# Optimization experiments

Measured on AMD Instinct MI355X. Metric: run time of the kernel, lower is better.

Reference implementation:

```python
import jax, jax.numpy as jnp
import numpy as np
import math

N_HEAD, D_HEAD, D_MODEL = 12, 64, 768
ATT_SPAN = 512            # max_position_embeddings // stride**block_index
SCALE_FACTOR = 3          # 1 + 2 (relative attention: content + c2p + p2c)
CLS_TOKENS = 1            # num_highway_cls_tokens + 1
INF = 1e6
LN_EPS = 1e-5
SCALE = 1.0 / (math.sqrt(D_HEAD) * math.sqrt(SCALE_FACTOR))


def setup_inputs() -> dict:
    key = jax.random.key(0)
    ks = jax.random.split(key, 10)
    B, S = 2, 2048
    lin = lambda k, shape: jax.random.normal(k, shape, dtype=jnp.float32) * 0.02
    return {
        "query": jax.random.normal(ks[0], (B, S, D_MODEL), dtype=jnp.float32),
        "attention_mask": jnp.ones((B, S), dtype=jnp.float32),
        "pos_key_embed": jax.random.normal(ks[1], (2 * ATT_SPAN, D_MODEL), dtype=jnp.float32),
        "pos_query_embed": jax.random.normal(ks[2], (2 * ATT_SPAN, D_MODEL), dtype=jnp.float32),
        "Wq": lin(ks[3], (N_HEAD * D_HEAD, D_MODEL)),
        "bq": jnp.zeros((N_HEAD * D_HEAD,), dtype=jnp.float32),
        "Wk": lin(ks[4], (N_HEAD * D_HEAD, D_MODEL)),
        "Wv": lin(ks[5], (D_MODEL, D_MODEL)),
        "bv": jnp.zeros((D_MODEL,), dtype=jnp.float32),
        "Wpq": lin(ks[6], (N_HEAD * D_HEAD, D_MODEL)),
        "bpq": jnp.zeros((N_HEAD * D_HEAD,), dtype=jnp.float32),
        "Wpk": lin(ks[7], (N_HEAD * D_HEAD, D_MODEL)),
        "r_w_bias": jax.random.normal(ks[8], (N_HEAD, D_HEAD), dtype=jnp.float32) * 0.02,
        "ln_gamma": jnp.ones((D_MODEL,), dtype=jnp.float32),
        "ln_beta": jnp.zeros((D_MODEL,), dtype=jnp.float32),
    }


def _forward(query, attention_mask, pos_key_embed, pos_query_embed,
             Wq, bq, Wk, Wv, bv, Wpq, bpq, Wpk, r_w_bias, ln_gamma, ln_beta):
    B, S, _ = query.shape
    # self-attention: key = value = query
    v = query @ Wv.T + bv                                             # v_head projection
    qh = (query @ Wq.T + bq).reshape(B, S, N_HEAD, D_HEAD)
    kh = (query @ Wk.T).reshape(B, S, N_HEAD, D_HEAD)
    vh = v.reshape(B, S, N_HEAD, D_MODEL // N_HEAD)
    qh = (qh + r_w_bias) * SCALE                                       # bias + scale fused into q

    content = jnp.einsum('bind,bjnd->bnij', qh, kh)                    # [B,n,S,S]

    # ---- disentangled relative-position bias (DeBERTa-style c2p + p2c) ----
    pos_k = (pos_key_embed @ Wpk.T).reshape(2 * ATT_SPAN, N_HEAD, D_HEAD).transpose(1, 0, 2)          # [n,2span,d]
    pos_q = (pos_query_embed @ Wpq.T + bpq).reshape(2 * ATT_SPAN, N_HEAD, D_HEAD).transpose(1, 0, 2)  # [n,2span,d]
    qbn = qh.transpose(0, 2, 1, 3)                                     # [B,n,S,d] (already scaled)
    kbn = kh.transpose(0, 2, 1, 3)
    rel = jnp.arange(S)[:, None] - jnp.arange(S)[None, :]              # [S,S] query - key

    # content -> position
    c2p = jnp.einsum('bnid,njd->bnij', qbn, pos_k)                     # [B,n,S,2span]
    c2p_idx = jnp.clip(rel + ATT_SPAN, 0, 2 * ATT_SPAN - 1)
    c2p_score = jnp.take_along_axis(c2p, c2p_idx[None, None], axis=-1) # [B,n,S,S]

    # position -> content
    p2c = jnp.einsum('bnjd,nid->bnji', kbn * (1.0 / math.sqrt(D_HEAD * SCALE_FACTOR)), pos_q)  # [B,n,S,2span]
    p2c_idx = jnp.clip(-rel + ATT_SPAN, 0, 2 * ATT_SPAN - 1)
    p2c_score = jnp.take_along_axis(p2c, p2c_idx[None, None], axis=-1).swapaxes(-1, -2)        # [B,n,S,S]

    bias = c2p_score + p2c_score
    # zero out bias on cls rows and cls columns (the padding/concat trick in the source)
    keep = (jnp.arange(S) >= CLS_TOKENS).astype(bias.dtype)
    bias = bias * (keep[:, None] * keep[None, :])

    score = content + bias
    score = score - INF * (1.0 - attention_mask[:, None, None, :])
    prob = jax.nn.softmax(score, axis=-1)                              # attention_dropout = 0.0

    attn_vec = jnp.einsum('bnij,bjnd->bind', prob, vh).reshape(B, S, D_MODEL)
    # fused residual + LayerNorm(attn_out)
    mu = attn_vec.mean(-1, keepdims=True)
    var = ((attn_vec - mu) ** 2).mean(-1, keepdims=True)
    ln = (attn_vec - mu) / jnp.sqrt(var + LN_EPS) * ln_gamma + ln_beta
    return query + ln


def reference(query, attention_mask, pos_key_embed, pos_query_embed,
              Wq, bq, Wk, Wv, bv, Wpq, bpq, Wpk, r_w_bias, ln_gamma, ln_beta):
    return _forward(query, attention_mask, pos_key_embed, pos_query_embed,
                    Wq, bq, Wk, Wv, bv, Wpq, bpq, Wpk, r_w_bias, ln_gamma, ln_beta)
```

## Files before the change

kernel.cpp:

```cpp
#include <hip/hip_runtime.h>
#include <math.h>

#define NB     2
#define SEQ    2048
#define NHEAD  12
#define DMODEL 768
#define SPAN2  1024
#define SCALEF 0.07216878364870323f

typedef unsigned short ushort;
typedef unsigned int   uint;
typedef __attribute__((ext_vector_type(8))) short  bh8;
typedef __attribute__((ext_vector_type(4))) float  f32x4;
typedef __attribute__((ext_vector_type(4))) unsigned short us4;

__device__ inline ushort f2bf(float x) {
    uint u = __builtin_bit_cast(uint, x);
    u += 0x7FFFu + ((u >> 16) & 1u);
    return (ushort)(u >> 16);
}
__device__ inline float b2f(ushort h) {
    uint u = ((uint)h) << 16;
    return __builtin_bit_cast(float, u);
}

__device__ __forceinline__ void gld16(const ushort* g, ushort* l) {
    __builtin_amdgcn_global_load_lds(
        (const __attribute__((address_space(1))) void*)g,
        (__attribute__((address_space(3))) void*)l, 16, 0, 0);
}

__device__ __forceinline__ bh8 ldsfrag(const ushort* tile, int row, int slot) {
    return *(const bh8*)((const char*)tile + row * 128 + (((slot ^ (row & 7)) << 4)));
}

struct CvtArgs {
    const float* src[8];
    ushort*      dst[8];
    int          n[8];
};

__global__ __launch_bounds__(256) void cvt_bf16(CvtArgs a)
{
    const int seg = blockIdx.y;
    const int i   = (blockIdx.x * 256 + threadIdx.x) * 8;
    if (i >= a.n[seg]) return;
    const float4* s = (const float4*)(a.src[seg] + i);
    const float4 x = s[0], y = s[1];
    bh8 o;
    o[0] = (short)f2bf(x.x); o[1] = (short)f2bf(x.y);
    o[2] = (short)f2bf(x.z); o[3] = (short)f2bf(x.w);
    o[4] = (short)f2bf(y.x); o[5] = (short)f2bf(y.y);
    o[6] = (short)f2bf(y.z); o[7] = (short)f2bf(y.w);
    *(bh8*)(a.dst[seg] + i) = o;
}

__global__ __launch_bounds__(256) void proj_mfma2(
    const ushort* __restrict__ X, const ushort* __restrict__ W,
    const float* __restrict__ b1, const float* __restrict__ b2,
    float scale, int rowsPerBatch,
    ushort* __restrict__ out, ushort* __restrict__ outT)
{
    __shared__ ushort Xs[32 * 64];
    __shared__ ushort Ws[64 * 64];
    const int r0 = blockIdx.x * 32;
    const int n  = blockIdx.y;
    const int c0 = n * 64;
    const int tid  = threadIdx.x;
    const int w    = tid >> 6;
    const int lane = tid & 63;
    const int lo   = lane & 15;
    const int hi8  = (lane >> 4) * 8;
    const int g4   = (lane >> 4) * 4;
    const int wr   = w & 1;
    const int wc   = w >> 1;
    const int r8   = lane >> 3;
    const int sl   = lane & 7;

    f32x4 acc[2] = {};
    for (int k0 = 0; k0 < DMODEL; k0 += 64) {
        {
            const int r = w * 8 + r8;
            const int s = sl ^ (r & 7);
            gld16(X + (size_t)(r0 + r) * DMODEL + k0 + s * 8, Xs + w * 512);
        }
        #pragma unroll
        for (int i = 0; i < 2; ++i) {
            const int c = i * 4 + w;
            const int r = c * 8 + r8;
            const int s = sl ^ (r & 7);
            gld16(W + (size_t)(c0 + r) * DMODEL + k0 + s * 8, Ws + c * 512);
        }
        __syncthreads();
        const bh8 a0 = ldsfrag(Xs, wr * 16 + lo, hi8 >> 3);
        const bh8 a1 = ldsfrag(Xs, wr * 16 + lo, 4 + (hi8 >> 3));
        #pragma unroll
        for (int ct = 0; ct < 2; ++ct) {
            const int row = wc * 32 + ct * 16 + lo;
            const bh8 wb0 = ldsfrag(Ws, row, hi8 >> 3);
            const bh8 wb1 = ldsfrag(Ws, row, 4 + (hi8 >> 3));
            acc[ct] = __builtin_amdgcn_mfma_f32_16x16x32_bf16(a0, wb0, acc[ct], 0, 0, 0);
            acc[ct] = __builtin_amdgcn_mfma_f32_16x16x32_bf16(a1, wb1, acc[ct], 0, 0, 0);
        }
        __syncthreads();
    }

    const int rbase = r0 + wr * 16 + g4;
    const int bb  = rbase / rowsPerBatch;
    const int rr0 = rbase - bb * rowsPerBatch;
    #pragma unroll
    for (int ct = 0; ct < 2; ++ct) {
        const int d = wc * 32 + ct * 16 + lo;
        const int c = c0 + d;
        const float badd = (b1 ? b1[c] : 0.f) + (b2 ? b2[c] : 0.f);
        if (out) {
            #pragma unroll
            for (int reg = 0; reg < 4; ++reg)
                out[(((size_t)bb * NHEAD + n) * rowsPerBatch + rr0 + reg) * 64 + d] =
                    f2bf((acc[ct][reg] + badd) * scale);
        }
        if (outT) {
            us4 o;
            #pragma unroll
            for (int reg = 0; reg < 4; ++reg)
                o[reg] = f2bf((acc[ct][reg] + badd) * scale);
            *(us4*)&outT[(((size_t)bb * NHEAD + n) * 64 + d) * rowsPerBatch + rr0] = o;
        }
    }
}

__global__ __launch_bounds__(256, 3) void attn_mfma8(
    const ushort* __restrict__ qh, const ushort* __restrict__ kh,
    const ushort* __restrict__ vht, const ushort* __restrict__ posk,
    const ushort* __restrict__ posq, const float* __restrict__ mask,
    float* __restrict__ attn)
{
    __shared__ ushort POS[128 * 64];
    __shared__ ushort Kb [64 * 64];
    __shared__ ushort Vb [64 * 64];
    __shared__ ushort T1c[64 * 68];
    __shared__ ushort T2c[64 * 68];

    const int id   = blockIdx.x;
    const int xcd  = id & 7;
    const int slot = id >> 3;
    const int bn   = xcd * 3 + (slot >> 5);
    const int i0   = (slot & 31) * 64;
    const int b    = bn / NHEAD;
    const int n    = bn % NHEAD;

    const int tid  = threadIdx.x;
    const int w    = tid >> 6;
    const int lane = tid & 63;
    const int lo   = lane & 15;
    const int hi8  = (lane >> 4) * 8;
    const int g4   = (lane >> 4) * 4;
    const int w16  = w * 16;
    const int r8   = lane >> 3;
    const int sl   = lane & 7;
    const int slotA = hi8 >> 3;

    const ushort* qrow = qh + ((size_t)bn * SEQ + i0 + w16 + lo) * 64;
    const bh8 qa0 = *(const bh8*)&qrow[hi8];
    const bh8 qa1 = *(const bh8*)&qrow[32 + hi8];

    const ushort* khb = kh   + (size_t)bn * SEQ * 64;
    const ushort* vtb = vht  + (size_t)bn * 64 * SEQ;
    const ushort* pkh = posk + (size_t)n * SPAN2 * 64;
    const ushort* pqh = posq + (size_t)n * SPAN2 * 64;
    const float*  mrw = mask + (size_t)b * SEQ;

    f32x4 accPV[4] = {};
    float mrow[4] = {-1e30f, -1e30f, -1e30f, -1e30f};
    float lrow[4] = {0.f, 0.f, 0.f, 0.f};

    for (int j0 = 0; j0 < SEQ; j0 += 64) {
        const int d0base = i0 - j0 + 449;

        #pragma unroll
        for (int i = 0; i < 2; ++i) {
            const int c = i * 4 + w;
            const int r = c * 8 + r8;
            const int s = sl ^ (r & 7);
            gld16(khb + (size_t)(j0 + r) * 64 + s * 8, Kb + c * 512);
        }
        #pragma unroll
        for (int i = 0; i < 4; ++i) {
            const int c = i * 4 + w;
            const int r = c * 8 + r8;
            const int s = sl ^ (r & 7);
            int gr = d0base + r; gr = gr < 0 ? 0 : (gr > SPAN2 - 1 ? SPAN2 - 1 : gr);
            gld16(pkh + (size_t)gr * 64 + s * 8, POS + c * 512);
        }
        __syncthreads();

        const bh8 ka0 = ldsfrag(Kb, w16 + lo, slotA);
        const bh8 ka1 = ldsfrag(Kb, w16 + lo, 4 + slotA);
        f32x4 z1[5];
        #pragma unroll
        for (int q = 0; q < 5; ++q) {
            const int u1 = (w + q) * 16 + lo;
            const bh8 pk0 = ldsfrag(POS, u1, slotA);
            const bh8 pk1 = ldsfrag(POS, u1, 4 + slotA);
            f32x4 a = {};
            a = __builtin_amdgcn_mfma_f32_16x16x32_bf16(qa0, pk0, a, 0, 0, 0);
            z1[q] = __builtin_amdgcn_mfma_f32_16x16x32_bf16(qa1, pk1, a, 0, 0, 0);
        }
        __syncthreads();

        #pragma unroll
        for (int i = 0; i < 4; ++i) {
            const int c = i * 4 + w;
            const int r = c * 8 + r8;
            const int s = sl ^ (r & 7);
            int gr = d0base + r; gr = gr < 0 ? 0 : (gr > SPAN2 - 1 ? SPAN2 - 1 : gr);
            gld16(pqh + (size_t)gr * 64 + s * 8, POS + c * 512);
        }
        #pragma unroll
        for (int i = 0; i < 2; ++i) {
            const int c = i * 4 + w;
            const int r = c * 8 + r8;
            const int s = sl ^ (r & 7);
            gld16(vtb + (size_t)r * SEQ + j0 + s * 8, Vb + c * 512);
        }
        #pragma unroll
        for (int q = 0; q < 5; ++q)
            #pragma unroll
            for (int reg = 0; reg < 4; ++reg) {
                const int cc2 = q * 16 + lo - g4 - reg;
                if (cc2 >= 0 && cc2 < 64)
                    T1c[(w16 + g4 + reg) * 68 + cc2] = f2bf(z1[q][reg]);
            }
        f32x4 accS[4];
        #pragma unroll
        for (int ct = 0; ct < 4; ++ct) {
            const bh8 kb0 = ldsfrag(Kb, ct * 16 + lo, slotA);
            const bh8 kb1 = ldsfrag(Kb, ct * 16 + lo, 4 + slotA);
            f32x4 z = {};
            z = __builtin_amdgcn_mfma_f32_16x16x32_bf16(qa0, kb0, z, 0, 0, 0);
            accS[ct] = __builtin_amdgcn_mfma_f32_16x16x32_bf16(qa1, kb1, z, 0, 0, 0);
        }
        float maskadd[4];
        #pragma unroll
        for (int ct = 0; ct < 4; ++ct)
            maskadd[ct] = -1e6f * (1.f - mrw[j0 + ct * 16 + lo]);
        __syncthreads();

        #pragma unroll
        for (int q = 0; q < 5; ++q) {
            const int u2 = (3 - w + q) * 16 + lo;
            const bh8 pq0 = ldsfrag(POS, u2, slotA);
            const bh8 pq1 = ldsfrag(POS, u2, 4 + slotA);
            f32x4 z = {};
            z = __builtin_amdgcn_mfma_f32_16x16x32_bf16(ka0, pq0, z, 0, 0, 0);
            z = __builtin_amdgcn_mfma_f32_16x16x32_bf16(ka1, pq1, z, 0, 0, 0);
            #pragma unroll
            for (int reg = 0; reg < 4; ++reg) {
                const int il2 = q * 16 + lo + g4 + reg - 15;
                if (il2 >= 0 && il2 < 64)
                    T2c[(w16 + g4 + reg) * 68 + il2] = f2bf(z[reg]);
            }
        }
        __syncthreads();

        float corr[4];
        char* pbase = (char*)POS + w * 2048;
        #pragma unroll
        for (int reg = 0; reg < 4; ++reg) {
            const int il = w16 + g4 + reg;
            const int gi = i0 + il;
            float s[4], rmax = -1e30f;
            #pragma unroll
            for (int ct = 0; ct < 4; ++ct) {
                const int jl = ct * 16 + lo;
                float v = accS[ct][reg];
                if (gi >= 1 && (j0 + jl) >= 1)
                    v += b2f(T1c[il * 68 + 63 - jl]) + b2f(T2c[jl * 68 + il]);
                v += maskadd[ct];
                s[ct] = v;
                rmax = fmaxf(rmax, v);
            }
            rmax = fmaxf(rmax, __shfl_xor(rmax, 1));
            rmax = fmaxf(rmax, __shfl_xor(rmax, 2));
            rmax = fmaxf(rmax, __shfl_xor(rmax, 4));
            rmax = fmaxf(rmax, __shfl_xor(rmax, 8));
            const float mnew = fmaxf(mrow[reg], rmax);
            const float cc   = __expf(mrow[reg] - mnew);
            float psum = 0.f;
            const int prow = g4 + reg;
            #pragma unroll
            for (int ct = 0; ct < 4; ++ct) {
                const float p = __expf(s[ct] - mnew);
                psum += p;
                *(ushort*)(pbase + prow * 128 + ((((ct * 16 + lo) * 2)) ^ ((prow & 7) * 16))) = f2bf(p);
            }
            psum += __shfl_xor(psum, 1);
            psum += __shfl_xor(psum, 2);
            psum += __shfl_xor(psum, 4);
            psum += __shfl_xor(psum, 8);
            lrow[reg] = lrow[reg] * cc + psum;
            mrow[reg] = mnew;
            corr[reg] = cc;
        }

        {
            const bh8 pa0 = *(const bh8*)(pbase + lo * 128 + ((slotA << 4) ^ ((lo & 7) * 16)));
            const bh8 pa1 = *(const bh8*)(pbase + lo * 128 + (((4 + slotA) << 4) ^ ((lo & 7) * 16)));
            #pragma unroll
            for (int dt = 0; dt < 4; ++dt) {
                const bh8 vb0 = ldsfrag(Vb, dt * 16 + lo, slotA);
                const bh8 vb1 = ldsfrag(Vb, dt * 16 + lo, 4 + slotA);
                f32x4 a = accPV[dt];
                #pragma unroll
                for (int reg = 0; reg < 4; ++reg) a[reg] *= corr[reg];
                a = __builtin_amdgcn_mfma_f32_16x16x32_bf16(pa0, vb0, a, 0, 0, 0);
                accPV[dt] = __builtin_amdgcn_mfma_f32_16x16x32_bf16(pa1, vb1, a, 0, 0, 0);
            }
        }
        __syncthreads();
    }

    #pragma unroll
    for (int reg = 0; reg < 4; ++reg) {
        const int i = i0 + w16 + g4 + reg;
        const float inv = 1.f / lrow[reg];
        #pragma unroll
        for (int dt = 0; dt < 4; ++dt)
            attn[((size_t)b * SEQ + i) * DMODEL + n * 64 + dt * 16 + lo] =
                accPV[dt][reg] * inv;
    }
}

__global__ __launch_bounds__(256) void resid_ln(
    float* __restrict__ attn, const float* __restrict__ query,
    const float* __restrict__ gamma, const float* __restrict__ beta)
{
    const int b = blockIdx.y;
    const int i = blockIdx.x;
    const size_t base = ((size_t)b * SEQ + i) * DMODEL;
    const int tid = threadIdx.x;

    float x[3];
    #pragma unroll
    for (int s = 0; s < 3; ++s) x[s] = attn[base + s * 256 + tid];

    float sum = x[0] + x[1] + x[2];
    float sq  = x[0]*x[0] + x[1]*x[1] + x[2]*x[2];
    #pragma unroll
    for (int off = 32; off; off >>= 1) {
        sum += __shfl_xor(sum, off);
        sq  += __shfl_xor(sq, off);
    }
    __shared__ float red[2][4];
    const int w = tid >> 6;
    if ((tid & 63) == 0) { red[0][w] = sum; red[1][w] = sq; }
    __syncthreads();
    sum = red[0][0] + red[0][1] + red[0][2] + red[0][3];
    sq  = red[1][0] + red[1][1] + red[1][2] + red[1][3];

    const float mu  = sum * (1.f / DMODEL);
    const float var = sq * (1.f / DMODEL) - mu * mu;
    const float inv = rsqrtf(var + 1e-5f);

    #pragma unroll
    for (int s = 0; s < 3; ++s) {
        const int c = s * 256 + tid;
        attn[base + c] = query[base + c] + (x[s] - mu) * inv * gamma[c] + beta[c];
    }
}

extern "C" void kernel_launch(void* const* d_in, const int* in_sizes, int n_in,
                              void* d_out, int out_size, void* d_ws, size_t ws_size,
                              hipStream_t stream)
{
    const float* query = (const float*)d_in[0];
    const float* mask  = (const float*)d_in[1];
    const float* pke   = (const float*)d_in[2];
    const float* pqe   = (const float*)d_in[3];
    const float* Wq    = (const float*)d_in[4];
    const float* bq    = (const float*)d_in[5];
    const float* Wk    = (const float*)d_in[6];
    const float* Wv    = (const float*)d_in[7];
    const float* bv    = (const float*)d_in[8];
    const float* Wpq   = (const float*)d_in[9];
    const float* bpq   = (const float*)d_in[10];
    const float* Wpk   = (const float*)d_in[11];
    const float* rwb   = (const float*)d_in[12];
    const float* gamma = (const float*)d_in[13];
    const float* beta  = (const float*)d_in[14];

    float* out = (float*)d_out;

    const int Q_N  = NB * SEQ * DMODEL;
    const int P_N  = SPAN2 * DMODEL;
    const int W_N  = DMODEL * DMODEL;
    const size_t QKV_ELEMS = (size_t)NB * NHEAD * SEQ * 64;
    const size_t POS_ELEMS = (size_t)NHEAD * SPAN2 * 64;

    ushort* xb   = (ushort*)d_ws;
    ushort* pkeb = xb   + Q_N;
    ushort* pqeb = pkeb + P_N;
    ushort* wqb  = pqeb + P_N;
    ushort* wkb  = wqb  + W_N;
    ushort* wvb  = wkb  + W_N;
    ushort* wpqb = wvb  + W_N;
    ushort* wpkb = wpqb + W_N;
    ushort* qh   = wpkb + W_N;
    ushort* kh   = qh   + QKV_ELEMS;
    ushort* vht  = kh   + QKV_ELEMS;
    ushort* pkp  = vht  + QKV_ELEMS;
    ushort* pqp  = pkp  + POS_ELEMS;

    dim3 blk(256);

    CvtArgs ca;
    ca.src[0] = query; ca.dst[0] = xb;   ca.n[0] = Q_N;
    ca.src[1] = pke;   ca.dst[1] = pkeb; ca.n[1] = P_N;
    ca.src[2] = pqe;   ca.dst[2] = pqeb; ca.n[2] = P_N;
    ca.src[3] = Wq;    ca.dst[3] = wqb;  ca.n[3] = W_N;
    ca.src[4] = Wk;    ca.dst[4] = wkb;  ca.n[4] = W_N;
    ca.src[5] = Wv;    ca.dst[5] = wvb;  ca.n[5] = W_N;
    ca.src[6] = Wpq;   ca.dst[6] = wpqb; ca.n[6] = W_N;
    ca.src[7] = Wpk;   ca.dst[7] = wpkb; ca.n[7] = W_N;
    cvt_bf16<<<dim3((Q_N / 8 + 255) / 256, 8), blk, 0, stream>>>(ca);

    proj_mfma2<<<dim3(128, NHEAD), blk, 0, stream>>>(xb,   wqb,  bq,  rwb, SCALEF, SEQ,   qh,  nullptr);
    proj_mfma2<<<dim3(128, NHEAD), blk, 0, stream>>>(xb,   wkb,  nullptr, nullptr, 1.f, SEQ, kh, nullptr);
    proj_mfma2<<<dim3(128, NHEAD), blk, 0, stream>>>(xb,   wvb,  bv,  nullptr, 1.f,   SEQ,   nullptr, vht);
    proj_mfma2<<<dim3(32,  NHEAD), blk, 0, stream>>>(pkeb, wpkb, nullptr, nullptr, 1.f, SPAN2, pkp, nullptr);
    proj_mfma2<<<dim3(32,  NHEAD), blk, 0, stream>>>(pqeb, wpqb, bpq, nullptr, SCALEF, SPAN2, pqp, nullptr);

    attn_mfma8<<<dim3(NB * NHEAD * (SEQ / 64)), blk, 0, stream>>>(
        qh, kh, vht, pkp, pqp, mask, out);

    resid_ln<<<dim3(SEQ, NB), blk, 0, stream>>>(out, query, gamma, beta);
}
```

Before: 245.5 us.

## Fuse QKV and positional projections; add clamped-tile fast path in attention

Measured after the change: 222.7 us. 1.1x faster.

```diff
diff --git a/kernel.cpp b/kernel.cpp
--- a/kernel.cpp
+++ b/kernel.cpp
@@ -55,14 +55,18 @@
     *(bh8*)(a.dst[seg] + i) = o;
 }
 
-__global__ __launch_bounds__(256) void proj_mfma2(
-    const ushort* __restrict__ X, const ushort* __restrict__ W,
-    const float* __restrict__ b1, const float* __restrict__ b2,
-    float scale, int rowsPerBatch,
-    ushort* __restrict__ out, ushort* __restrict__ outT)
+__global__ __launch_bounds__(256) void proj_qkv(
+    const ushort* __restrict__ X,
+    const ushort* __restrict__ Wq, const ushort* __restrict__ Wk,
+    const ushort* __restrict__ Wv,
+    const float* __restrict__ bq, const float* __restrict__ rwb,
+    const float* __restrict__ bv,
+    ushort* __restrict__ qh, ushort* __restrict__ kh, ushort* __restrict__ vht)
 {
-    __shared__ ushort Xs[32 * 64];
-    __shared__ ushort Ws[64 * 64];
+    __shared__ ushort Xs [32 * 64];
+    __shared__ ushort Wqs[64 * 64];
+    __shared__ ushort Wks[64 * 64];
+    __shared__ ushort Wvs[64 * 64];
     const int r0 = blockIdx.x * 32;
     const int n  = blockIdx.y;
     const int c0 = n * 64;
@@ -76,8 +80,9 @@
     const int wc   = w >> 1;
     const int r8   = lane >> 3;
     const int sl   = lane & 7;
-
-    f32x4 acc[2] = {};
+    const int slotA = hi8 >> 3;
+
+    f32x4 aq[2] = {}, ak[2] = {}, av[2] = {};
     for (int k0 = 0; k0 < DMODEL; k0 += 64) {
         {
             const int r = w * 8 + r8;
@@ -89,47 +94,120 @@
             const int c = i * 4 + w;
             const int r = c * 8 + r8;
             const int s = sl ^ (r & 7);
-            gld16(W + (size_t)(c0 + r) * DMODEL + k0 + s * 8, Ws + c * 512);
-        }
-        __syncthreads();
-        const bh8 a0 = ldsfrag(Xs, wr * 16 + lo, hi8 >> 3);
-        const bh8 a1 = ldsfrag(Xs, wr * 16 + lo, 4 + (hi8 >> 3));
+            gld16(Wq + (size_t)(c0 + r) * DMODEL + k0 + s * 8, Wqs + c * 512);
+            gld16(Wk + (size_t)(c0 + r) * DMODEL + k0 + s * 8, Wks + c * 512);
+            gld16(Wv + (size_t)(c0 + r) * DMODEL + k0 + s * 8, Wvs + c * 512);
+        }
+        __syncthreads();
+        const bh8 a0 = ldsfrag(Xs, wr * 16 + lo, slotA);
+        const bh8 a1 = ldsfrag(Xs, wr * 16 + lo, 4 + slotA);
         #pragma unroll
         for (int ct = 0; ct < 2; ++ct) {
             const int row = wc * 32 + ct * 16 + lo;
-            const bh8 wb0 = ldsfrag(Ws, row, hi8 >> 3);
-            const bh8 wb1 = ldsfrag(Ws, row, 4 + (hi8 >> 3));
-            acc[ct] = __builtin_amdgcn_mfma_f32_16x16x32_bf16(a0, wb0, acc[ct], 0, 0, 0);
-            acc[ct] = __builtin_amdgcn_mfma_f32_16x16x32_bf16(a1, wb1, acc[ct], 0, 0, 0);
+            aq[ct] = __builtin_amdgcn_mfma_f32_16x16x32_bf16(a0, ldsfrag(Wqs, row, slotA),     aq[ct], 0, 0, 0);
+            aq[ct] = __builtin_amdgcn_mfma_f32_16x16x32_bf16(a1, ldsfrag(Wqs, row, 4 + slotA), aq[ct], 0, 0, 0);
+            ak[ct] = __builtin_amdgcn_mfma_f32_16x16x32_bf16(a0, ldsfrag(Wks, row, slotA),     ak[ct], 0, 0, 0);
+            ak[ct] = __builtin_amdgcn_mfma_f32_16x16x32_bf16(a1, ldsfrag(Wks, row, 4 + slotA), ak[ct], 0, 0, 0);
+            av[ct] = __builtin_amdgcn_mfma_f32_16x16x32_bf16(a0, ldsfrag(Wvs, row, slotA),     av[ct], 0, 0, 0);
+            av[ct] = __builtin_amdgcn_mfma_f32_16x16x32_bf16(a1, ldsfrag(Wvs, row, 4 + slotA), av[ct], 0, 0, 0);
         }
         __syncthreads();
     }
 
     const int rbase = r0 + wr * 16 + g4;
-    const int bb  = rbase / rowsPerBatch;
-    const int rr0 = rbase - bb * rowsPerBatch;
+    const int bb  = rbase >> 11;
+    const int rr0 = rbase & (SEQ - 1);
     #pragma unroll
     for (int ct = 0; ct < 2; ++ct) {
         const int d = wc * 32 + ct * 16 + lo;
         const int c = c0 + d;
-        const float badd = (b1 ? b1[c] : 0.f) + (b2 ? b2[c] : 0.f);
-        if (out) {
-            #pragma unroll
-            for (int reg = 0; reg < 4; ++reg)
-                out[(((size_t)bb * NHEAD + n) * rowsPerBatch + rr0 + reg) * 64 + d] =
-                    f2bf((acc[ct][reg] + badd) * scale);
-        }
-        if (outT) {
-            us4 o;
-            #pragma unroll
-            for (int reg = 0; reg < 4; ++reg)
-                o[reg] = f2bf((acc[ct][reg] + badd) * scale);
-            *(us4*)&outT[(((size_t)bb * NHEAD + n) * 64 + d) * rowsPerBatch + rr0] = o;
-        }
-    }
-}
-
-__global__ __launch_bounds__(256, 3) void attn_mfma8(
+        const float bqv = bq[c] + rwb[c];
+        const float bvv = bv[c];
+        us4 o;
+        #pragma unroll
+        for (int reg = 0; reg < 4; ++reg) {
+            const size_t rowi = ((size_t)bb * NHEAD + n) * SEQ + rr0 + reg;
+            qh[rowi * 64 + d] = f2bf((aq[ct][reg] + bqv) * SCALEF);
+            kh[rowi * 64 + d] = f2bf(ak[ct][reg]);
+            o[reg] = f2bf(av[ct][reg] + bvv);
+        }
+        *(us4*)&vht[(((size_t)bb * NHEAD + n) * 64 + d) * SEQ + rr0] = o;
+    }
+}
+
+__global__ __launch_bounds__(256) void proj_pos(
+    const ushort* __restrict__ PKe, const ushort* __restrict__ PQe,
+    const ushort* __restrict__ Wpk, const ushort* __restrict__ Wpq,
+    const float* __restrict__ bpq,
+    ushort* __restrict__ pkp, ushort* __restrict__ pqp)
+{
+    __shared__ ushort Xk [32 * 64];
+    __shared__ ushort Xq [32 * 64];
+    __shared__ ushort Wks[64 * 64];
+    __shared__ ushort Wqs[64 * 64];
+    const int r0 = blockIdx.x * 32;
+    const int n  = blockIdx.y;
+    const int c0 = n * 64;
+    const int tid  = threadIdx.x;
+    const int w    = tid >> 6;
+    const int lane = tid & 63;
+    const int lo   = lane & 15;
+    const int hi8  = (lane >> 4) * 8;
+    const int g4   = (lane >> 4) * 4;
+    const int wr   = w & 1;
+    const int wc   = w >> 1;
+    const int r8   = lane >> 3;
+    const int sl   = lane & 7;
+    const int slotA = hi8 >> 3;
+
+    f32x4 apk[2] = {}, apq[2] = {};
+    for (int k0 = 0; k0 < DMODEL; k0 += 64) {
+        {
+            const int r = w * 8 + r8;
+            const int s = sl ^ (r & 7);
+            gld16(PKe + (size_t)(r0 + r) * DMODEL + k0 + s * 8, Xk + w * 512);
+            gld16(PQe + (size_t)(r0 + r) * DMODEL + k0 + s * 8, Xq + w * 512);
+        }
+        #pragma unroll
+        for (int i = 0; i < 2; ++i) {
+            const int c = i * 4 + w;
+            const int r = c * 8 + r8;
+            const int s = sl ^ (r & 7);
+            gld16(Wpk + (size_t)(c0 + r) * DMODEL + k0 + s * 8, Wks + c * 512);
+            gld16(Wpq + (size_t)(c0 + r) * DMODEL + k0 + s * 8, Wqs + c * 512);
+        }
+        __syncthreads();
+        const bh8 xk0 = ldsfrag(Xk, wr * 16 + lo, slotA);
+        const bh8 xk1 = ldsfrag(Xk, wr * 16 + lo, 4 + slotA);
+        const bh8 xq0 = ldsfrag(Xq, wr * 16 + lo, slotA);
+        const bh8 xq1 = ldsfrag(Xq, wr * 16 + lo, 4 + slotA);
+        #pragma unroll
+        for (int ct = 0; ct < 2; ++ct) {
+            const int row = wc * 32 + ct * 16 + lo;
+            apk[ct] = __builtin_amdgcn_mfma_f32_16x16x32_bf16(xk0, ldsfrag(Wks, row, slotA),     apk[ct], 0, 0, 0);
+            apk[ct] = __builtin_amdgcn_mfma_f32_16x16x32_bf16(xk1, ldsfrag(Wks, row, 4 + slotA), apk[ct], 0, 0, 0);
+            apq[ct] = __builtin_amdgcn_mfma_f32_16x16x32_bf16(xq0, ldsfrag(Wqs, row, slotA),     apq[ct], 0, 0, 0);
+            apq[ct] = __builtin_amdgcn_mfma_f32_16x16x32_bf16(xq1, ldsfrag(Wqs, row, 4 + slotA), apq[ct], 0, 0, 0);
+        }
+        __syncthreads();
+    }
+
+    const int rr0 = r0 + wr * 16 + g4;
+    #pragma unroll
+    for (int ct = 0; ct < 2; ++ct) {
+        const int d = wc * 32 + ct * 16 + lo;
+        const int c = c0 + d;
+        const float badd = bpq[c];
+        #pragma unroll
+        for (int reg = 0; reg < 4; ++reg) {
+            const size_t rowi = ((size_t)n * SPAN2 + rr0 + reg);
+            pkp[rowi * 64 + d] = f2bf(apk[ct][reg]);
+            pqp[rowi * 64 + d] = f2bf((apq[ct][reg] + badd) * SCALEF);
+        }
+    }
+}
+
+__global__ __launch_bounds__(256, 3) void attn_mfma9(
     const ushort* __restrict__ qh, const ushort* __restrict__ kh,
     const ushort* __restrict__ vht, const ushort* __restrict__ posk,
     const ushort* __restrict__ posq, const float* __restrict__ mask,
@@ -140,6 +218,8 @@
     __shared__ ushort Vb [64 * 64];
     __shared__ ushort T1c[64 * 68];
     __shared__ ushort T2c[64 * 68];
+    __shared__ ushort CL [8 * 64];
+    __shared__ float  Crow[2][64];
 
     const int id   = blockIdx.x;
     const int xcd  = id & 7;
@@ -170,13 +250,44 @@
     const ushort* pqh = posq + (size_t)n * SPAN2 * 64;
     const float*  mrw = mask + (size_t)b * SEQ;
 
+    if (w == 0) {
+        const int row = lane >> 3;
+        const int sr  = row & 3;
+        const ushort* src = (sr == 0) ? pkh
+                          : (sr == 1) ? pkh + (size_t)(SPAN2 - 1) * 64
+                          : (sr == 2) ? pqh
+                          :             pqh + (size_t)(SPAN2 - 1) * 64;
+        gld16(src + (lane & 7) * 8, CL);
+    }
+    __syncthreads();
+    {
+        const bh8 p0a = *(const bh8*)&CL[0 * 64 + hi8];
+        const bh8 p0b = *(const bh8*)&CL[0 * 64 + 32 + hi8];
+        const bh8 p1a = *(const bh8*)&CL[1 * 64 + hi8];
+        const bh8 p1b = *(const bh8*)&CL[1 * 64 + 32 + hi8];
+        float c0p = 0.f, c1p = 0.f;
+        #pragma unroll
+        for (int e = 0; e < 8; ++e) {
+            const float q0 = b2f((ushort)qa0[e]);
+            const float q1 = b2f((ushort)qa1[e]);
+            c0p += q0 * b2f((ushort)p0a[e]) + q1 * b2f((ushort)p0b[e]);
+            c1p += q0 * b2f((ushort)p1a[e]) + q1 * b2f((ushort)p1b[e]);
+        }
+        c0p += __shfl_xor(c0p, 16); c0p += __shfl_xor(c0p, 32);
+        c1p += __shfl_xor(c1p, 16); c1p += __shfl_xor(c1p, 32);
+        if (hi8 == 0) { Crow[0][w16 + lo] = c0p; Crow[1][w16 + lo] = c1p; }
+    }
+
     f32x4 accPV[4] = {};
     float mrow[4] = {-1e30f, -1e30f, -1e30f, -1e30f};
     float lrow[4] = {0.f, 0.f, 0.f, 0.f};
 
     for (int j0 = 0; j0 < SEQ; j0 += 64) {
         const int d0base = i0 - j0 + 449;
-
+        const bool clamp0 = (d0base <= -126);
+        const bool clamp1 = (d0base >= 1023);
+
+        if (!clamp0 && !clamp1) {
         #pragma unroll
         for (int i = 0; i < 2; ++i) {
             const int c = i * 4 + w;
@@ -318,6 +429,110 @@
             }
         }
         __syncthreads();
+
+        } else {
+        #pragma unroll
+        for (int i = 0; i < 2; ++i) {
+            const int c = i * 4 + w;
+            const int r = c * 8 + r8;
+            const int s = sl ^ (r & 7);
+            gld16(khb + (size_t)(j0 + r) * 64 + s * 8, Kb + c * 512);
+            gld16(vtb + (size_t)r * SEQ + j0 + s * 8, Vb + c * 512);
+        }
+        __syncthreads();
+
+        const int clrow = clamp0 ? 2 : 3;
+        float pqf0[8], pqf1[8];
+        {
+            const bh8 pa = *(const bh8*)&CL[clrow * 64 + hi8];
+            const bh8 pb = *(const bh8*)&CL[clrow * 64 + 32 + hi8];
+            #pragma unroll
+            for (int e = 0; e < 8; ++e) {
+                pqf0[e] = b2f((ushort)pa[e]);
+                pqf1[e] = b2f((ushort)pb[e]);
+            }
+        }
+
+        f32x4 accS[4];
+        float Dv[4];
+        #pragma unroll
+        for (int ct = 0; ct < 4; ++ct) {
+            const bh8 kb0 = ldsfrag(Kb, ct * 16 + lo, slotA);
+            const bh8 kb1 = ldsfrag(Kb, ct * 16 + lo, 4 + slotA);
+            f32x4 z = {};
+            z = __builtin_amdgcn_mfma_f32_16x16x32_bf16(qa0, kb0, z, 0, 0, 0);
+            accS[ct] = __builtin_amdgcn_mfma_f32_16x16x32_bf16(qa1, kb1, z, 0, 0, 0);
+            float p = 0.f;
+            #pragma unroll
+            for (int e = 0; e < 8; ++e)
+                p += b2f((ushort)kb0[e]) * pqf0[e] + b2f((ushort)kb1[e]) * pqf1[e];
+            p += __shfl_xor(p, 16);
+            p += __shfl_xor(p, 32);
+            Dv[ct] = p;
+        }
+        float maskadd[4];
+        #pragma unroll
+        for (int ct = 0; ct < 4; ++ct)
+            maskadd[ct] = -1e6f * (1.f - mrw[j0 + ct * 16 + lo]);
+
+        float corr[4];
+        char* pbase = (char*)POS + w * 2048;
+        const float* crw = Crow[clamp0 ? 0 : 1];
+        #pragma unroll
+        for (int reg = 0; reg < 4; ++reg) {
+            const int il = w16 + g4 + reg;
+            const int gi = i0 + il;
+            const float Cv = crw[il];
+            float s[4], rmax = -1e30f;
+            #pragma unroll
+            for (int ct = 0; ct < 4; ++ct) {
+                const int jl = ct * 16 + lo;
+                float v = accS[ct][reg];
+                if (gi >= 1 && (j0 + jl) >= 1)
+                    v += Cv + Dv[ct];
+                v += maskadd[ct];
+                s[ct] = v;
+                rmax = fmaxf(rmax, v);
+            }
+            rmax = fmaxf(rmax, __shfl_xor(rmax, 1));
+            rmax = fmaxf(rmax, __shfl_xor(rmax, 2));
+            rmax = fmaxf(rmax, __shfl_xor(rmax, 4));
+            rmax = fmaxf(rmax, __shfl_xor(rmax, 8));
+            const float mnew = fmaxf(mrow[reg], rmax);
+            const float cc   = __expf(mrow[reg] - mnew);
+            float psum = 0.f;
+            const int prow = g4 + reg;
+            #pragma unroll
+            for (int ct = 0; ct < 4; ++ct) {
+                const float p = __expf(s[ct] - mnew);
+                psum += p;
+                *(ushort*)(pbase + prow * 128 + ((((ct * 16 + lo) * 2)) ^ ((prow & 7) * 16))) = f2bf(p);
+            }
+            psum += __shfl_xor(psum, 1);
+            psum += __shfl_xor(psum, 2);
+            psum += __shfl_xor(psum, 4);
+            psum += __shfl_xor(psum, 8);
+            lrow[reg] = lrow[reg] * cc + psum;
+            mrow[reg] = mnew;
+            corr[reg] = cc;
+        }
+
+        {
+            const bh8 pa0 = *(const bh8*)(pbase + lo * 128 + ((slotA << 4) ^ ((lo & 7) * 16)));
+            const bh8 pa1 = *(const bh8*)(pbase + lo * 128 + (((4 + slotA) << 4) ^ ((lo & 7) * 16)));
+            #pragma unroll
+            for (int dt = 0; dt < 4; ++dt) {
+                const bh8 vb0 = ldsfrag(Vb, dt * 16 + lo, slotA);
+                const bh8 vb1 = ldsfrag(Vb, dt * 16 + lo, 4 + slotA);
+                f32x4 a = accPV[dt];
+                #pragma unroll
+                for (int reg = 0; reg < 4; ++reg) a[reg] *= corr[reg];
+                a = __builtin_amdgcn_mfma_f32_16x16x32_bf16(pa0, vb0, a, 0, 0, 0);
+                accPV[dt] = __builtin_amdgcn_mfma_f32_16x16x32_bf16(pa1, vb1, a, 0, 0, 0);
+            }
+        }
+        __syncthreads();
+        }
     }
 
     #pragma unroll
@@ -424,13 +639,12 @@
     ca.src[7] = Wpk;   ca.dst[7] = wpkb; ca.n[7] = W_N;
     cvt_bf16<<<dim3((Q_N / 8 + 255) / 256, 8), blk, 0, stream>>>(ca);
 
-    proj_mfma2<<<dim3(128, NHEAD), blk, 0, stream>>>(xb,   wqb,  bq,  rwb, SCALEF, SEQ,   qh,  nullptr);
-    proj_mfma2<<<dim3(128, NHEAD), blk, 0, stream>>>(xb,   wkb,  nullptr, nullptr, 1.f, SEQ, kh, nullptr);
-    proj_mfma2<<<dim3(128, NHEAD), blk, 0, stream>>>(xb,   wvb,  bv,  nullptr, 1.f,   SEQ,   nullptr, vht);
-    proj_mfma2<<<dim3(32,  NHEAD), blk, 0, stream>>>(pkeb, wpkb, nullptr, nullptr, 1.f, SPAN2, pkp, nullptr);
-    proj_mfma2<<<dim3(32,  NHEAD), blk, 0, stream>>>(pqeb, wpqb, bpq, nullptr, SCALEF, SPAN2, pqp, nullptr);
-
-    attn_mfma8<<<dim3(NB * NHEAD * (SEQ / 64)), blk, 0, stream>>>(
+    proj_qkv<<<dim3(NB * SEQ / 32, NHEAD), blk, 0, stream>>>(
+        xb, wqb, wkb, wvb, bq, rwb, bv, qh, kh, vht);
+    proj_pos<<<dim3(SPAN2 / 32, NHEAD), blk, 0, stream>>>(
+        pkeb, pqeb, wpkb, wpqb, bpq, pkp, pqp);
+
+    attn_mfma9<<<dim3(NB * NHEAD * (SEQ / 64)), blk, 0, stream>>>(
         qh, kh, vht, pkp, pqp, mask, out);
 
     resid_ln<<<dim3(SEQ, NB), blk, 0, stream>>>(out, query, gamma, beta);
```
